# Kernel tuning notes

Measured on AMD Instinct MI355X. Metric: run time of the kernel, lower is better.

## Reference

```python
import jax, jax.numpy as jnp
from jax import lax
import numpy as np

N_CLASS = 5
B, T = 2048, 2048


def setup_inputs() -> dict:
    key = jax.random.key(0)
    k1, k2 = jax.random.split(key)
    x = jax.random.normal(k1, (B, T, N_CLASS), dtype=jnp.float32)
    mask = jnp.ones((B, T), dtype=jnp.int32)
    transform = jax.random.normal(k2, (N_CLASS + 2, N_CLASS + 2), dtype=jnp.float32)
    return {"x": x, "mask": mask, "transform": transform}


def reference(x, mask, transform):
    # Batched Viterbi decode. x:[B,T,C], mask:[B,T], transform:[C+2,C+2]
    Bb, Tt, C = x.shape
    START, END = C, C + 1
    trans = transform[:C, :C]                      # [C,C] prev -> curr
    mb = mask.astype(bool)

    dp0 = x[:, 0, :] + transform[START, :C][None]  # [B,C]

    def step(dp, inp):
        xt, mt = inp                               # xt:[B,C], mt:[B]
        sc = dp[:, :, None] + trans[None]          # [B,C_prev,C_curr]
        bp = jnp.argmax(sc, axis=1)                # [B,C]
        new_dp = jnp.max(sc, axis=1) + xt          # [B,C]
        dp_out = jnp.where(mt[:, None], new_dp, dp)
        # identity backpointer on padded steps so backtrace is a no-op there
        bp_out = jnp.where(mt[:, None], bp, jnp.arange(C)[None, :])
        return dp_out, bp_out

    xs = (jnp.moveaxis(x[:, 1:, :], 1, 0),         # [T-1,B,C]
          jnp.moveaxis(mb[:, 1:], 1, 0))           # [T-1,B]
    dp, bps = lax.scan(step, dp0, xs)              # bps: [T-1,B,C]

    final = dp + transform[:C, END][None]          # [B,C]
    max_score = jnp.max(final, axis=1)             # [B]
    last = jnp.argmax(final, axis=1)               # [B]

    def back(idx, bp):
        prev = jnp.take_along_axis(bp, idx[:, None], axis=1)[:, 0]
        return prev, idx

    first, rest = lax.scan(back, last, bps, reverse=True)  # rest: [T-1,B]
    path = jnp.concatenate([first[None], rest], axis=0)    # [T,B]
    return max_score, path.T                                # [B], [B,T]
```

## Files before the change

kernel.cpp:

```cpp
#include <hip/hip_runtime.h>
#include <cstdint>

#define B_    2048
#define T_    2048
#define TD    7
#define IDENT 0x4688u

__device__ __forceinline__ uint32_t mcompose(uint32_t f, uint32_t g) {
    uint32_t r = 0;
#pragma unroll
    for (int j = 0; j < 5; ++j) {
        uint32_t gj = (g >> (3 * j)) & 7u;
        r |= ((f >> (3 * gj)) & 7u) << (3 * j);
    }
    return r;
}

__device__ __forceinline__ uint32_t cvtpk(float lo, float hi) {
    uint32_t r;
    asm("v_cvt_pk_bf16_f32 %0, %1, %2" : "=v"(r) : "v"(lo), "v"(hi));
    return r;
}

__device__ __forceinline__ float xget(const uint32_t* w, int h) {
    return (h & 1) ? __uint_as_float(w[h >> 1] & 0xFFFF0000u)
                   : __uint_as_float(w[h >> 1] << 16);
}

__device__ __forceinline__ int gidx(int cc, int q) {
    int s = q + (cc & 7);
    s = (s >= 20) ? s - 20 : s;
    return 20 * cc + s;
}

template<bool P>
__device__ __forceinline__ void hstep(const uint32_t* w, int base, bool pred,
                                      float (&dp)[5], const float (&tr)[5][5]) {
    float nd[5];
#pragma unroll
    for (int j = 0; j < 5; ++j) {
        float v = fmaxf(fmaxf(fmaxf(fmaxf(dp[0] + tr[0][j], dp[1] + tr[1][j]),
                                    dp[2] + tr[2][j]), dp[3] + tr[3][j]),
                        dp[4] + tr[4][j]);
        nd[j] = v + xget(w, base + j);
    }
#pragma unroll
    for (int j = 0; j < 5; ++j) dp[j] = (P && !pred) ? dp[j] : nd[j];
}

template<bool SEL>
__device__ __forceinline__ uint32_t lstep(const uint32_t* w, int base, bool mm,
                                          float (&dp)[5], const float (&tr)[5][5],
                                          uint32_t& rho) {
    float nd[5]; int aa[5]; uint32_t pk = 0;
#pragma unroll
    for (int j = 0; j < 5; ++j) {
        float s[5];
#pragma unroll
        for (int i = 0; i < 5; ++i) {
            float f = dp[i] + tr[i][j];
            s[i] = __uint_as_float((__float_as_uint(f) & ~7u) | (uint32_t)(7 - i));
        }
        float m = fmaxf(fmaxf(fmaxf(fmaxf(s[0], s[1]), s[2]), s[3]), s[4]);
        int a = 7 - (int)(__float_as_uint(m) & 7u);
        float v = m + xget(w, base + j);
        if (SEL) { a = mm ? a : j; nd[j] = mm ? v : dp[j]; }
        else     { nd[j] = v; }
        aa[j] = a;
        pk |= ((uint32_t)a) << (3 * j);
    }
    uint32_t nr = 0;
#pragma unroll
    for (int j = 0; j < 5; ++j) nr |= ((rho >> (3 * aa[j])) & 7u) << (3 * j);
    rho = nr;
#pragma unroll
    for (int j = 0; j < 5; ++j) dp[j] = nd[j];
    return pk;
}

__global__ __launch_bounds__(64) void k_all(
    const float* __restrict__ x, const int* __restrict__ mask,
    const float* __restrict__ tf, float* __restrict__ out)
{
    __shared__ __align__(16) uint16_t xs[10240];
    const int b = blockIdx.x, c = threadIdx.x;

    const float4* gx = (const float4*)(x + (size_t)b * (T_ * 5));
    const int*    gi = mask + (size_t)b * T_;

#pragma unroll
    for (int qi = 0; qi < 40; ++qi) {
        int fi = c + 64 * qi;
        float4 v = gx[fi];
        uint32_t e0 = 4u * (uint32_t)fi;
        uint32_t co = e0 / 160u;
        uint32_t el = e0 - 160u * co;
        uint32_t q  = el >> 3;
        uint32_t s  = q + (co & 7u); s = (s >= 20u) ? s - 20u : s;
        uint32_t ha = 160u * co + 8u * s + (el & 7u);
        uint2 p; p.x = cvtpk(v.x, v.y); p.y = cvtpk(v.z, v.w);
        *(uint2*)(xs + ha) = p;
    }

    uint32_t mb = 0;
    {
        int mv[32];
#pragma unroll
        for (int q = 0; q < 32; ++q) mv[q] = gi[c + 64 * q];
#pragma unroll
        for (int q = 0; q < 32; ++q) {
            unsigned long long bal = __ballot(mv[q] != 0);
            if (c == 2 * q)     mb = (uint32_t)bal;
            if (c == 2 * q + 1) mb = (uint32_t)(bal >> 32);
        }
    }

    float tr[5][5], ts[5], te[5];
#pragma unroll
    for (int i = 0; i < 5; ++i)
#pragma unroll
        for (int j = 0; j < 5; ++j) tr[i][j] = tf[i * TD + j];
#pragma unroll
    for (int j = 0; j < 5; ++j) ts[j] = tf[5 * TD + j];
#pragma unroll
    for (int j = 0; j < 5; ++j) te[j] = tf[j * TD + 6];

    const bool allm = __all(mb == 0xFFFFFFFFu);
    uint32_t mh = __shfl_up(mb, 1);
    mh = (c > 0) ? (mh >> 24) : 0u;

    __syncthreads();

    const uint4* xsv = (const uint4*)xs;
    const int hc = (c > 0) ? c - 1 : 0;

    uint32_t hw[20];
#pragma unroll
    for (int k = 0; k < 5; ++k) {
        uint4 t = xsv[gidx(hc, 15 + k)];
        hw[4*k] = t.x; hw[4*k+1] = t.y; hw[4*k+2] = t.z; hw[4*k+3] = t.w;
    }
    float dp[5];
#pragma unroll
    for (int j = 0; j < 5; ++j) dp[j] = xget(hw, j);
    if (allm) {
#pragma unroll
        for (int h = 1; h <= 7; ++h) hstep<false>(hw, 5 * h, true, dp, tr);
    } else {
#pragma unroll
        for (int h = 1; h <= 7; ++h) hstep<true>(hw, 5 * h, ((mh >> h) & 1u) != 0, dp, tr);
    }
    if (c == 0) {
        uint4 t0 = xsv[gidx(0, 0)];
        uint32_t w0[4] = { t0.x, t0.y, t0.z, t0.w };
#pragma unroll
        for (int j = 0; j < 5; ++j) dp[j] = xget(w0, j) + ts[j];
    }
    float dpE[5];
#pragma unroll
    for (int j = 0; j < 5; ++j) dpE[j] = (c == 0) ? 0.0f : dp[j];

    uint32_t acc[16];
    uint32_t rho = IDENT;
#pragma unroll
    for (int bb = 0; bb < 4; ++bb) {
        uint32_t w[20];
#pragma unroll
        for (int k = 0; k < 5; ++k) {
            uint4 t = xsv[gidx(c, 5 * bb + k)];
            w[4*k] = t.x; w[4*k+1] = t.y; w[4*k+2] = t.z; w[4*k+3] = t.w;
        }
#pragma unroll
        for (int ll = 0; ll < 8; ++ll) {
            const int l = 8 * bb + ll;
            uint32_t pk;
            if (l == 0) {
                bool mm = (c != 0) && ((mb & 1u) != 0);
                pk = lstep<true>(w, 0, mm, dp, tr, rho);
            } else if (allm) {
                pk = lstep<false>(w, 5 * ll, true, dp, tr, rho);
            } else {
                pk = lstep<true>(w, 5 * ll, ((mb >> l) & 1u) != 0, dp, tr, rho);
            }
            if (l & 1) acc[l >> 1] |= pk << 16;
            else       acc[l >> 1]  = pk;
        }
    }

    float svec[5];
#pragma unroll
    for (int j = 0; j < 5; ++j) {
        int r = (rho >> (3 * j)) & 7;
        float e = dpE[0];
        e = (r == 1) ? dpE[1] : e;
        e = (r == 2) ? dpE[2] : e;
        e = (r == 3) ? dpE[3] : e;
        e = (r == 4) ? dpE[4] : e;
        svec[j] = dp[j] - e;
    }

    uint32_t I = rho;
#pragma unroll
    for (int d = 1; d < 64; d <<= 1) {
        uint32_t oth = __shfl_down(I, d);
        uint32_t cm  = mcompose(I, oth);
        I = (c + d < 64) ? cm : I;
    }
    float best = dp[0] + te[0]; int lastv = 0;
#pragma unroll
    for (int j = 1; j < 5; ++j) {
        float s = dp[j] + te[j];
        if (s > best) { best = s; lastv = j; }
    }
    const int last = __shfl(lastv, 63);
    uint32_t M = __shfl_down(I, 1);
    M = (c < 63) ? M : IDENT;
    const int ec = (M >> (3 * last)) & 7;

    {
        float v = svec[0];
        v = (ec == 1) ? svec[1] : v;
        v = (ec == 2) ? svec[2] : v;
        v = (ec == 3) ? svec[3] : v;
        v = (ec == 4) ? svec[4] : v;
        if (c == 63) v += te[last];
#pragma unroll
        for (int off = 1; off < 64; off <<= 1) v += __shfl_xor(v, off);
        if (c == 0) out[b] = v;
    }

    float pv[32];
    int e = ec;
#pragma unroll
    for (int l = 31; l >= 0; --l) {
        pv[l] = (float)e;
        uint32_t p = (acc[l >> 1] >> (16 * (l & 1))) & 0xFFFFu;
        e = (p >> (3 * e)) & 7;
    }
    float* path = out + B_ + (size_t)b * T_ + c * 32;
#pragma unroll
    for (int q = 0; q < 8; ++q) {
        float4 v; v.x = pv[4*q]; v.y = pv[4*q+1]; v.z = pv[4*q+2]; v.w = pv[4*q+3];
        ((float4*)path)[q] = v;
    }
}

extern "C" void kernel_launch(void* const* d_in, const int* in_sizes, int n_in,
                              void* d_out, int out_size, void* d_ws, size_t ws_size,
                              hipStream_t stream) {
    const float* x         = (const float*)d_in[0];
    const int*   mask      = (const int*)d_in[1];
    const float* transform = (const float*)d_in[2];
    float*       out       = (float*)d_out;

    hipLaunchKernelGGL(k_all, dim3(B_), dim3(64), 0, stream,
                       x, mask, transform, out);
}
```

Measured before the change: 36.48 us.

## Split each sequence across two wavefronts with 16-step chunks per thread

Doubles the block to 128 threads so each thread handles 16 timesteps instead of 32, halving the serial per-thread max-plus chain and backtrace. The cross-wave prefix of backpointer maps and the score reduction now pass through shared memory with extra barriers, and the shared-memory layout and its swizzle are redone for the smaller chunks. Mask loading changes from ballots to vectorized int4 reads per thread. The halo warm-up is still 7 steps, which is now a larger fraction of each thread's work.

```diff
diff --git a/kernel.cpp b/kernel.cpp
--- a/kernel.cpp
+++ b/kernel.cpp
@@ -4,6 +4,7 @@
 #define B_    2048
 #define T_    2048
 #define TD    7
+#define NCHK  128
 #define IDENT 0x4688u
 
 __device__ __forceinline__ uint32_t mcompose(uint32_t f, uint32_t g) {
@@ -28,9 +29,9 @@
 }
 
 __device__ __forceinline__ int gidx(int cc, int q) {
-    int s = q + (cc & 7);
-    s = (s >= 20) ? s - 20 : s;
-    return 20 * cc + s;
+    int s = q + ((cc >> 2) & 7);
+    s = (s >= 10) ? s - 10 : s;
+    return 10 * cc + s;
 }
 
 template<bool P>
@@ -78,40 +79,47 @@
     return pk;
 }
 
-__global__ __launch_bounds__(64) void k_all(
+__global__ __launch_bounds__(128) void k_all(
     const float* __restrict__ x, const int* __restrict__ mask,
     const float* __restrict__ tf, float* __restrict__ out)
 {
     __shared__ __align__(16) uint16_t xs[10240];
+    __shared__ uint32_t tot[2];
+    __shared__ float    part[2];
+    __shared__ int      lastS;
+    uint32_t* xs32 = (uint32_t*)xs;
+
     const int b = blockIdx.x, c = threadIdx.x;
+    const int lane = c & 63, w = c >> 6;
 
     const float4* gx = (const float4*)(x + (size_t)b * (T_ * 5));
-    const int*    gi = mask + (size_t)b * T_;
-
-#pragma unroll
-    for (int qi = 0; qi < 40; ++qi) {
-        int fi = c + 64 * qi;
+
+#pragma unroll
+    for (int qi = 0; qi < 20; ++qi) {
+        int fi = c + 128 * qi;
         float4 v = gx[fi];
         uint32_t e0 = 4u * (uint32_t)fi;
-        uint32_t co = e0 / 160u;
-        uint32_t el = e0 - 160u * co;
+        uint32_t co = e0 / 80u;
+        uint32_t el = e0 - 80u * co;
         uint32_t q  = el >> 3;
-        uint32_t s  = q + (co & 7u); s = (s >= 20u) ? s - 20u : s;
-        uint32_t ha = 160u * co + 8u * s + (el & 7u);
+        uint32_t s  = q + ((co >> 2) & 7u); s = (s >= 10u) ? s - 10u : s;
+        uint32_t dA = 4u * (10u * co + s) + ((el >> 1) & 3u);
         uint2 p; p.x = cvtpk(v.x, v.y); p.y = cvtpk(v.z, v.w);
-        *(uint2*)(xs + ha) = p;
+        *(uint2*)(xs32 + dA) = p;
     }
 
     uint32_t mb = 0;
     {
-        int mv[32];
-#pragma unroll
-        for (int q = 0; q < 32; ++q) mv[q] = gi[c + 64 * q];
-#pragma unroll
-        for (int q = 0; q < 32; ++q) {
-            unsigned long long bal = __ballot(mv[q] != 0);
-            if (c == 2 * q)     mb = (uint32_t)bal;
-            if (c == 2 * q + 1) mb = (uint32_t)(bal >> 32);
+        const int4* gmc = (const int4*)(mask + (size_t)b * T_ + 16 * c);
+        int4 m[4];
+#pragma unroll
+        for (int u = 0; u < 4; ++u) m[u] = gmc[u];
+#pragma unroll
+        for (int u = 0; u < 4; ++u) {
+            mb |= (m[u].x ? 1u : 0u) << (4 * u);
+            mb |= (m[u].y ? 1u : 0u) << (4 * u + 1);
+            mb |= (m[u].z ? 1u : 0u) << (4 * u + 2);
+            mb |= (m[u].w ? 1u : 0u) << (4 * u + 3);
         }
     }
 
@@ -125,19 +133,29 @@
 #pragma unroll
     for (int j = 0; j < 5; ++j) te[j] = tf[j * TD + 6];
 
-    const bool allm = __all(mb == 0xFFFFFFFFu);
     uint32_t mh = __shfl_up(mb, 1);
-    mh = (c > 0) ? (mh >> 24) : 0u;
-
-    __syncthreads();
-
-    const uint4* xsv = (const uint4*)xs;
+    if (lane == 0 && w == 1) mh = 0;
+    if (c == 64) {
+        const int4* gp = (const int4*)(mask + (size_t)b * T_ + 16 * 63);
+        int4 m2 = gp[2], m3 = gp[3];
+        uint32_t hb = 0;
+        hb |= (m2.x ? 1u : 0u) << 8;  hb |= (m2.y ? 1u : 0u) << 9;
+        hb |= (m2.z ? 1u : 0u) << 10; hb |= (m2.w ? 1u : 0u) << 11;
+        hb |= (m3.x ? 1u : 0u) << 12; hb |= (m3.y ? 1u : 0u) << 13;
+        hb |= (m3.z ? 1u : 0u) << 14; hb |= (m3.w ? 1u : 0u) << 15;
+        mh = hb;
+    }
+    mh = (c > 0) ? (mh >> 8) : 0u;
+
+    const int allm = __syncthreads_and(mb == 0xFFFFu);
+
+    const uint4* xsv = (const uint4*)xs32;
     const int hc = (c > 0) ? c - 1 : 0;
 
     uint32_t hw[20];
 #pragma unroll
     for (int k = 0; k < 5; ++k) {
-        uint4 t = xsv[gidx(hc, 15 + k)];
+        uint4 t = xsv[gidx(hc, 5 + k)];
         hw[4*k] = t.x; hw[4*k+1] = t.y; hw[4*k+2] = t.z; hw[4*k+3] = t.w;
     }
     float dp[5];
@@ -160,15 +178,15 @@
 #pragma unroll
     for (int j = 0; j < 5; ++j) dpE[j] = (c == 0) ? 0.0f : dp[j];
 
-    uint32_t acc[16];
+    uint32_t acc[8];
     uint32_t rho = IDENT;
 #pragma unroll
-    for (int bb = 0; bb < 4; ++bb) {
-        uint32_t w[20];
+    for (int bb = 0; bb < 2; ++bb) {
+        uint32_t wv[20];
 #pragma unroll
         for (int k = 0; k < 5; ++k) {
             uint4 t = xsv[gidx(c, 5 * bb + k)];
-            w[4*k] = t.x; w[4*k+1] = t.y; w[4*k+2] = t.z; w[4*k+3] = t.w;
+            wv[4*k] = t.x; wv[4*k+1] = t.y; wv[4*k+2] = t.z; wv[4*k+3] = t.w;
         }
 #pragma unroll
         for (int ll = 0; ll < 8; ++ll) {
@@ -176,11 +194,11 @@
             uint32_t pk;
             if (l == 0) {
                 bool mm = (c != 0) && ((mb & 1u) != 0);
-                pk = lstep<true>(w, 0, mm, dp, tr, rho);
+                pk = lstep<true>(wv, 0, mm, dp, tr, rho);
             } else if (allm) {
-                pk = lstep<false>(w, 5 * ll, true, dp, tr, rho);
+                pk = lstep<false>(wv, 5 * ll, true, dp, tr, rho);
             } else {
-                pk = lstep<true>(w, 5 * ll, ((mb >> l) & 1u) != 0, dp, tr, rho);
+                pk = lstep<true>(wv, 5 * ll, ((mb >> l) & 1u) != 0, dp, tr, rho);
             }
             if (l & 1) acc[l >> 1] |= pk << 16;
             else       acc[l >> 1]  = pk;
@@ -204,18 +222,25 @@
     for (int d = 1; d < 64; d <<= 1) {
         uint32_t oth = __shfl_down(I, d);
         uint32_t cm  = mcompose(I, oth);
-        I = (c + d < 64) ? cm : I;
-    }
-    float best = dp[0] + te[0]; int lastv = 0;
-#pragma unroll
-    for (int j = 1; j < 5; ++j) {
-        float s = dp[j] + te[j];
-        if (s > best) { best = s; lastv = j; }
-    }
-    const int last = __shfl(lastv, 63);
-    uint32_t M = __shfl_down(I, 1);
-    M = (c < 63) ? M : IDENT;
-    const int ec = (M >> (3 * last)) & 7;
+        I = (lane + d < 64) ? cm : I;
+    }
+    if (lane == 0) tot[w] = I;
+    if (c == NCHK - 1) {
+        float best = dp[0] + te[0]; int last = 0;
+#pragma unroll
+        for (int j = 1; j < 5; ++j) {
+            float s = dp[j] + te[j];
+            if (s > best) { best = s; last = j; }
+        }
+        lastS = last;
+    }
+    __syncthreads();
+
+    uint32_t Tw = (w == 0) ? tot[1] : IDENT;
+    uint32_t Ex = __shfl_down(I, 1);
+    uint32_t M  = (lane < 63) ? mcompose(Ex, Tw) : Tw;
+    const int last = lastS;
+    const int ec = (int)((M >> (3 * last)) & 7u);
 
     {
         float v = svec[0];
@@ -223,23 +248,25 @@
         v = (ec == 2) ? svec[2] : v;
         v = (ec == 3) ? svec[3] : v;
         v = (ec == 4) ? svec[4] : v;
-        if (c == 63) v += te[last];
+        if (c == NCHK - 1) v += te[last];
 #pragma unroll
         for (int off = 1; off < 64; off <<= 1) v += __shfl_xor(v, off);
-        if (c == 0) out[b] = v;
-    }
-
-    float pv[32];
+        if (lane == 0) part[w] = v;
+    }
+    __syncthreads();
+    if (c == 0) out[b] = part[0] + part[1];
+
+    float pv[16];
     int e = ec;
 #pragma unroll
-    for (int l = 31; l >= 0; --l) {
+    for (int l = 15; l >= 0; --l) {
         pv[l] = (float)e;
         uint32_t p = (acc[l >> 1] >> (16 * (l & 1))) & 0xFFFFu;
         e = (p >> (3 * e)) & 7;
     }
-    float* path = out + B_ + (size_t)b * T_ + c * 32;
-#pragma unroll
-    for (int q = 0; q < 8; ++q) {
+    float* path = out + B_ + (size_t)b * T_ + 16 * c;
+#pragma unroll
+    for (int q = 0; q < 4; ++q) {
         float4 v; v.x = pv[4*q]; v.y = pv[4*q+1]; v.z = pv[4*q+2]; v.w = pv[4*q+3];
         ((float4*)path)[q] = v;
     }
@@ -253,6 +280,6 @@
     const float* transform = (const float*)d_in[2];
     float*       out       = (float*)d_out;
 
-    hipLaunchKernelGGL(k_all, dim3(B_), dim3(64), 0, stream,
+    hipLaunchKernelGGL(k_all, dim3(B_), dim3(128), 0, stream,
                        x, mask, transform, out);
 }
```

After: 40.35 us. 10.6% more time.
